# Kernel tuning notes

Measured on AMD Instinct MI355X. Metric: run time of the kernel, lower is better.

## Reference

```python
import jax, jax.numpy as jnp
import numpy as np

B, C, H, W = 64, 512, 7, 7        # x4: dim_b=512, layer4 spatial 7x7
HY, WY = 28, 28                   # y (x1): layer1 56x56 -> cov1 stride2 -> 28x28
NUM_HEADS = 8
HEAD_DIM = C // NUM_HEADS
SCALE = HEAD_DIM ** -0.5
K1, K2 = 2, 3
LN_EPS = 1e-5


def _avgpool_same(y, k, p):
    # torch nn.AvgPool2d(kernel=k, stride=1, padding=p), count_include_pad=True
    s = jax.lax.reduce_window(y, 0.0, jax.lax.add, (1, 1, k, k), (1, 1, 1, 1),
                              [(0, 0), (0, 0), (p, p), (p, p)])
    return s / float(k * k)


def setup_inputs() -> dict:
    key = jax.random.key(0)
    ks = jax.random.split(key, 8)
    x = jax.random.normal(ks[0], (B, C, H, W), dtype=jnp.float32)
    y = jax.random.normal(ks[1], (B, C, HY, WY), dtype=jnp.float32)
    # Linear weights stored as [in, out] (apply via x @ W)
    Wq = jax.random.normal(ks[2], (C, C), dtype=jnp.float32) * 0.02
    Wkv = jax.random.normal(ks[3], (C, 2 * C), dtype=jnp.float32) * 0.02
    Wproj = jax.random.normal(ks[4], (C, C), dtype=jnp.float32) * 0.02
    bproj = jnp.zeros((C,), dtype=jnp.float32)
    gamma = jnp.ones((C,), dtype=jnp.float32)
    beta = jnp.zeros((C,), dtype=jnp.float32)
    attn_w1 = jnp.full((1,), 0.5, dtype=jnp.float32)
    attn_w2 = jnp.full((1,), 0.5, dtype=jnp.float32)
    return dict(x=x, y=y, Wq=Wq, Wkv=Wkv, Wproj=Wproj, bproj=bproj,
                gamma=gamma, beta=beta, attn_w1=attn_w1, attn_w2=attn_w2)


def _topk_masked_softmax(attn, kc):
    # torch: scatter top-kc indices into a 0/1 mask, then where(mask>0, attn, -inf).
    # Equivalent (tie-free, as with continuous random logits): keep entries >= kth value.
    thr = jax.lax.top_k(attn, kc)[0][..., -1:]
    masked = jnp.where(attn >= jax.lax.stop_gradient(thr), attn, -jnp.inf)
    return jax.nn.softmax(masked, axis=-1)


def reference(x, y, Wq, Wkv, Wproj, bproj, gamma, beta, attn_w1, attn_w2):
    # Multi-scale pooling on y (all stride 1, 'same' spatial size)
    y = _avgpool_same(y, 3, 1) + _avgpool_same(y, 5, 2) + _avgpool_same(y, 7, 3)
    N1 = HY * WY
    y = y.reshape(B, C, N1).transpose(0, 2, 1)          # [B, N1, C]
    # LayerNorm over C
    mu = jnp.mean(y, axis=-1, keepdims=True)
    var = jnp.var(y, axis=-1, keepdims=True)
    y = (y - mu) / jnp.sqrt(var + LN_EPS) * gamma + beta

    N = H * W
    xs = x.reshape(B, C, N).transpose(0, 2, 1)          # [B, N, C]

    kv = (y @ Wkv).reshape(B, N1, 2, NUM_HEADS, HEAD_DIM)
    kv = kv.transpose(2, 0, 3, 1, 4)                    # [2, B, h, N1, d]
    k, v = kv[0], kv[1]
    q = (xs @ Wq).reshape(B, N, NUM_HEADS, HEAD_DIM).transpose(0, 2, 1, 3)  # [B,h,N,d]

    attn = jnp.einsum('bhnd,bhmd->bhnm', q, k) * SCALE  # [B, h, N, N1]

    attn1 = _topk_masked_softmax(attn, N1 // K1)
    attn2 = _topk_masked_softmax(attn, N1 // K2)
    out1 = jnp.einsum('bhnm,bhmd->bhnd', attn1, v)
    out2 = jnp.einsum('bhnm,bhmd->bhnd', attn2, v)
    out = out1 * attn_w1 + out2 * attn_w2               # [B, h, N, d]

    out = out.transpose(0, 2, 1, 3).reshape(B, N, C)    # [B, N, C]
    out = out @ Wproj + bproj
    return out.transpose(0, 2, 1).reshape(B, C, H, W)
```

## Files before the change

### kernel.cpp

```cpp
#include <hip/hip_runtime.h>
#include <hip/hip_bf16.h>


typedef __hip_bfloat16 bf16;
using bf16x8 = __attribute__((ext_vector_type(8))) short;
using f32x4 = __attribute__((ext_vector_type(4))) float;

#define DI __device__ __forceinline__

DI unsigned short b2u(float f) {
  bf16 h = __float2bfloat16(f);
  return *reinterpret_cast<unsigned short*>(&h);
}
DI float u2f(short s) { return __uint_as_float(((unsigned int)(unsigned short)s) << 16); }

DI float unkey(unsigned int k) {
  unsigned int u = (k & 0x80000000u) ? (k & 0x7FFFFFFFu) : ~k;
  return __uint_as_float(u);
}

#define GLD_LDS16(g, l)                                                              \
  __builtin_amdgcn_global_load_lds((const __attribute__((address_space(1))) unsigned int*)(g), \
                                   (__attribute__((address_space(3))) unsigned int*)(l), 16, 0, 0)

__global__ __launch_bounds__(256) void prep_pool_kernel(
    const float* __restrict__ Wkv, const float* __restrict__ Wq, const float* __restrict__ Wproj,
    const float* __restrict__ x, const float* __restrict__ y, bf16* __restrict__ wkvT,
    bf16* __restrict__ wqT, bf16* __restrict__ wpT, bf16* __restrict__ xsTb,
    bf16* __restrict__ Vt, bf16* __restrict__ pooledT) {
  __shared__ __align__(16) unsigned char pMem[26912];
  const int blk = blockIdx.x;
  const int tid = threadIdx.x;
  if (blk < 1024) {
    float(*t)[33] = reinterpret_cast<float(*)[33]>(pMem);
    const float* W;
    bf16* WT;
    int N, bx, by;
    if (blk < 512) { W = Wkv; WT = wkvT; N = 1024; bx = blk & 31; by = blk >> 5; }
    else if (blk < 768) { W = Wq; WT = wqT; N = 512; bx = (blk - 512) & 15; by = (blk - 512) >> 4; }
    else { W = Wproj; WT = wpT; N = 512; bx = (blk - 768) & 15; by = (blk - 768) >> 4; }
    const int n0 = bx * 32, k0 = by * 32;
    for (int i = tid; i < 1024; i += 256) {
      int kr = i >> 5, nc = i & 31;
      t[kr][nc] = W[(size_t)(k0 + kr) * N + n0 + nc];
    }
    __syncthreads();
    for (int i = tid; i < 1024; i += 256) {
      int nr = i >> 5, kc = i & 31;
      WT[(size_t)(n0 + nr) * 512 + k0 + kc] = __float2bfloat16(t[kc][nr]);
    }
  } else if (blk < 1536) {
    float(*xt)[51] = reinterpret_cast<float(*)[51]>(pMem);
    const int q2 = blk - 1024;
    const int b = q2 >> 3, cg = q2 & 7;
    const float* xp = x + ((size_t)b * 512 + cg * 64) * 49;
    for (int i = tid; i < 3136; i += 256) {
      int cc = i / 49, r = i - cc * 49;
      xt[cc][r] = xp[i];
    }
    __syncthreads();
    for (int i = tid; i < 3136; i += 256) {
      int r = i >> 6, cc = i & 63;
      xsTb[((size_t)b * 49 + r) * 512 + cg * 64 + cc] = __float2bfloat16(xt[cc][r]);
    }
  } else if (blk < 3584) {
    int idx = (blk - 1536) * 256 + tid;
    int row = idx >> 4, c = idx & 15;
    Vt[(size_t)row * 800 + 784 + c] = __float2bfloat16(0.f);
  } else {
    float(*I)[841] = reinterpret_cast<float(*)[841]>(pMem);
    const int p = blk - 3584;
    const int wk = (p & 7) * 512 + (p >> 3);
    const int b = wk >> 6, cg = wk & 63;
    const float* srcb = y + ((size_t)b * 512 + cg * 8) * 784;
    bf16* drow = pooledT + ((size_t)b * 784) * 512 + cg * 8;
    for (int i = tid; i < 8 * 57; i += 256) {
      int q = i / 57, e = i - q * 57;
      I[q][(e < 29) ? e : (e - 28) * 29] = 0.f;
    }
    {
      const int w = tid >> 6, lane = tid & 63;
      const int hl = lane >> 5, c = lane & 31;
      const int pp = w * 2 + hl;
      if (c < 28) {
        const float* sp = srcb + (size_t)pp * 784;
        float run = 0.f;
        for (int r = 0; r < 28; ++r) {
          float v = sp[r * 28 + c];
#pragma unroll
          for (int d = 1; d < 28; d <<= 1) {
            float tt = __shfl_up(v, d, 32);
            if (c >= d) v += tt;
          }
          run += v;
          I[pp][(r + 1) * 29 + c + 1] = run;
        }
      }
    }
    __syncthreads();
    for (int j = tid; j < 784; j += 256) {
      int r = j / 28, c = j - (j / 28) * 28;
      int r0[3], r1[3], c0[3], c1[3];
#pragma unroll
      for (int pk = 1; pk <= 3; ++pk) {
        r0[pk - 1] = max(r - pk, 0) * 29;
        r1[pk - 1] = (min(r + pk, 27) + 1) * 29;
        c0[pk - 1] = max(c - pk, 0);
        c1[pk - 1] = min(c + pk, 27) + 1;
      }
      unsigned int u[4];
#pragma unroll
      for (int q = 0; q < 4; ++q) {
        float vv[2];
#pragma unroll
        for (int tt = 0; tt < 2; ++tt) {
          const float* Ip = I[q * 2 + tt];
          float acc = 0.f;
#pragma unroll
          for (int k = 0; k < 3; ++k) {
            float s = Ip[r1[k] + c1[k]] - Ip[r0[k] + c1[k]] - Ip[r1[k] + c0[k]] + Ip[r0[k] + c0[k]];
            acc += s * ((k == 0) ? (1.f / 9.f) : (k == 1) ? (1.f / 25.f) : (1.f / 49.f));
          }
          vv[tt] = acc;
        }
        u[q] = (unsigned int)b2u(vv[0]) | ((unsigned int)b2u(vv[1]) << 16);
      }
      *reinterpret_cast<uint4*>(drow + (size_t)j * 512) = make_uint4(u[0], u[1], u[2], u[3]);
    }
  }
}

__global__ __launch_bounds__(256) void ln_q_kernel(const bf16* __restrict__ pooledT,
                                                   const float* __restrict__ gamma,
                                                   const float* __restrict__ beta,
                                                   bf16* __restrict__ yln,
                                                   const bf16* __restrict__ A,
                                                   const bf16* __restrict__ Bt,
                                                   bf16* __restrict__ Qb) {
  __shared__ __align__(16) bf16 As[128 * 32];
  __shared__ __align__(16) bf16 Bs[128 * 32];
  const int blk = blockIdx.x;
  const int tid = threadIdx.x;
  if (blk < 100) {
    const int lane = tid & 63;
    const int w = tid >> 6, wr = w >> 1, wc = w & 1;
    const int m0 = (blk >> 2) * 128, n0 = (blk & 3) * 128;
    f32x4 acc[4][4];
#pragma unroll
    for (int m = 0; m < 4; ++m)
#pragma unroll
      for (int n = 0; n < 4; ++n) acc[m][n] = f32x4{0.f, 0.f, 0.f, 0.f};
    const int s0 = tid, s1 = tid + 256;
    const bf16* Ag0 = A + (size_t)(m0 + (s0 >> 2)) * 512 + (s0 & 3) * 8;
    const bf16* Ag1 = A + (size_t)(m0 + (s1 >> 2)) * 512 + (s1 & 3) * 8;
    const bf16* Bg0 = Bt + (size_t)(n0 + (s0 >> 2)) * 512 + (s0 & 3) * 8;
    const bf16* Bg1 = Bt + (size_t)(n0 + (s1 >> 2)) * 512 + (s1 & 3) * 8;
    bf16* Al0 = As + s0 * 8;
    bf16* Al1 = As + s1 * 8;
    bf16* Bl0 = Bs + s0 * 8;
    bf16* Bl1 = Bs + s1 * 8;
    const int fr = lane & 15;
    const int ko = (lane >> 4) * 8;
    const int rh = lane >> 4;
    for (int k0 = 0; k0 < 512; k0 += 32) {
      GLD_LDS16(Ag0 + k0, Al0);
      GLD_LDS16(Ag1 + k0, Al1);
      GLD_LDS16(Bg0 + k0, Bl0);
      GLD_LDS16(Bg1 + k0, Bl1);
      __syncthreads();
      bf16x8 af[4], bfr[4];
#pragma unroll
      for (int m = 0; m < 4; ++m)
        af[m] = *reinterpret_cast<const bf16x8*>(As + (wr * 64 + m * 16 + fr) * 32 + ko);
#pragma unroll
      for (int n = 0; n < 4; ++n)
        bfr[n] = *reinterpret_cast<const bf16x8*>(Bs + (wc * 64 + n * 16 + fr) * 32 + ko);
#pragma unroll
      for (int m = 0; m < 4; ++m)
#pragma unroll
        for (int n = 0; n < 4; ++n)
          acc[m][n] = __builtin_amdgcn_mfma_f32_16x16x32_bf16(af[m], bfr[n], acc[m][n], 0, 0, 0);
      __syncthreads();
    }
#pragma unroll
    for (int m = 0; m < 4; ++m) {
#pragma unroll
      for (int n = 0; n < 4; ++n) {
        int col = n0 + wc * 64 + n * 16 + fr;
        const size_t cbase = ((size_t)(col >> 6)) * (49 * 64) + (col & 63);
#pragma unroll
        for (int r = 0; r < 4; ++r) {
          int row = m0 + wr * 64 + m * 16 + rh * 4 + r;
          if (row < 3136) {
            int b = row / 49, rr = row - (row / 49) * 49;
            Qb[((size_t)b * 8) * (49 * 64) + cbase + (size_t)rr * 64] = __float2bfloat16(acc[m][n][r]);
          }
        }
      }
    }
  } else {
    const int row = (blk - 100) * 4 + (tid >> 6);
    const int lane = tid & 63;
    bf16x8 raw = *reinterpret_cast<const bf16x8*>(pooledT + (size_t)row * 512 + lane * 8);
    float v[8];
    float s = 0.f, s2 = 0.f;
#pragma unroll
    for (int j = 0; j < 8; ++j) {
      v[j] = u2f(raw[j]);
      s += v[j];
      s2 += v[j] * v[j];
    }
#pragma unroll
    for (int off = 32; off; off >>= 1) {
      s += __shfl_xor(s, off, 64);
      s2 += __shfl_xor(s2, off, 64);
    }
    float mu = s * (1.f / 512.f);
    float rs = rsqrtf(s2 * (1.f / 512.f) - mu * mu + 1e-5f);
    float4 g0 = *reinterpret_cast<const float4*>(gamma + lane * 8);
    float4 g1 = *reinterpret_cast<const float4*>(gamma + lane * 8 + 4);
    float4 e0 = *reinterpret_cast<const float4*>(beta + lane * 8);
    float4 e1 = *reinterpret_cast<const float4*>(beta + lane * 8 + 4);
    float gg[8] = {g0.x, g0.y, g0.z, g0.w, g1.x, g1.y, g1.z, g1.w};
    float bb[8] = {e0.x, e0.y, e0.z, e0.w, e1.x, e1.y, e1.z, e1.w};
    unsigned int u[4];
#pragma unroll
    for (int q = 0; q < 4; ++q) {
      float o0 = (v[2 * q] - mu) * rs * gg[2 * q] + bb[2 * q];
      float o1 = (v[2 * q + 1] - mu) * rs * gg[2 * q + 1] + bb[2 * q + 1];
      u[q] = (unsigned int)b2u(o0) | ((unsigned int)b2u(o1) << 16);
    }
    *reinterpret_cast<uint4*>(yln + (size_t)row * 512 + lane * 8) =
        make_uint4(u[0], u[1], u[2], u[3]);
  }
}

__global__ __launch_bounds__(256) void kv_mfma(const bf16* __restrict__ A,
                                               const bf16* __restrict__ Bt,
                                               bf16* __restrict__ Kb, bf16* __restrict__ Vt) {
  extern __shared__ __align__(16) bf16 smem[];
  bf16* As = smem;
  bf16* Bs = smem + 128 * 32;
  const int tid = threadIdx.x;
  const int lane = tid & 63;
  const int w = tid >> 6, wr = w >> 1, wc = w & 1;

  const int lin = blockIdx.y * 8 + blockIdx.x;
  const int c8 = lin & 7, j = lin >> 3;
  const int ex = j & 7, ey = c8 * 49 + (j >> 3);
  const int m0 = ey * 128, n0 = ex * 128;

  f32x4 acc[4][4];
#pragma unroll
  for (int m = 0; m < 4; ++m)
#pragma unroll
    for (int n = 0; n < 4; ++n) acc[m][n] = f32x4{0.f, 0.f, 0.f, 0.f};

  const int s0 = tid, s1 = tid + 256;
  const bf16* Ag0 = A + (size_t)(m0 + (s0 >> 2)) * 512 + (s0 & 3) * 8;
  const bf16* Ag1 = A + (size_t)(m0 + (s1 >> 2)) * 512 + (s1 & 3) * 8;
  const bf16* Bg0 = Bt + (size_t)(n0 + (s0 >> 2)) * 512 + (s0 & 3) * 8;
  const bf16* Bg1 = Bt + (size_t)(n0 + (s1 >> 2)) * 512 + (s1 & 3) * 8;
  bf16* Al0 = As + s0 * 8;
  bf16* Al1 = As + s1 * 8;
  bf16* Bl0 = Bs + s0 * 8;
  bf16* Bl1 = Bs + s1 * 8;

  const int fr = lane & 15;
  const int ko = (lane >> 4) * 8;
  const int rh = lane >> 4;

  for (int k0 = 0; k0 < 512; k0 += 32) {
    GLD_LDS16(Ag0 + k0, Al0);
    GLD_LDS16(Ag1 + k0, Al1);
    GLD_LDS16(Bg0 + k0, Bl0);
    GLD_LDS16(Bg1 + k0, Bl1);
    __syncthreads();
    bf16x8 af[4], bfr[4];
#pragma unroll
    for (int m = 0; m < 4; ++m)
      af[m] = *reinterpret_cast<const bf16x8*>(As + (wr * 64 + m * 16 + fr) * 32 + ko);
#pragma unroll
    for (int n = 0; n < 4; ++n)
      bfr[n] = *reinterpret_cast<const bf16x8*>(Bs + (wc * 64 + n * 16 + fr) * 32 + ko);
#pragma unroll
    for (int m = 0; m < 4; ++m)
#pragma unroll
      for (int n = 0; n < 4; ++n)
        acc[m][n] = __builtin_amdgcn_mfma_f32_16x16x32_bf16(af[m], bfr[n], acc[m][n], 0, 0, 0);
    __syncthreads();
  }

  if (n0 < 512) {
#pragma unroll
    for (int m = 0; m < 4; ++m) {
#pragma unroll
      for (int n = 0; n < 4; ++n) {
        int col = n0 + wc * 64 + n * 16 + fr;
        const size_t cbase = ((size_t)(col >> 6)) * (784 * 64) + (col & 63);
#pragma unroll
        for (int r = 0; r < 4; ++r) {
          int row = m0 + wr * 64 + m * 16 + rh * 4 + r;
          int b = row / 784, n1 = row - (row / 784) * 784;
          Kb[((size_t)b * 8) * (784 * 64) + cbase + (size_t)n1 * 64] = __float2bfloat16(acc[m][n][r]);
        }
      }
    }
  } else {
    bf16* stage = smem;
#pragma unroll
    for (int p = 0; p < 2; ++p) {
      __syncthreads();
      if (wr == p) {
#pragma unroll
        for (int m = 0; m < 4; ++m) {
#pragma unroll
          for (int n = 0; n < 4; ++n) {
            int coll = wc * 64 + n * 16 + fr;
            int rowl = m * 16 + rh * 4;
            unsigned int u0 = (unsigned int)b2u(acc[m][n][0]) | ((unsigned int)b2u(acc[m][n][1]) << 16);
            unsigned int u1 = (unsigned int)b2u(acc[m][n][2]) | ((unsigned int)b2u(acc[m][n][3]) << 16);
            *reinterpret_cast<uint2*>(stage + coll * 72 + rowl) = make_uint2(u0, u1);
          }
        }
      }
      __syncthreads();
      const int rbase = m0 + p * 64;
      for (int i = tid; i < 1024; i += 256) {
        int cc = i >> 3, tc = i & 7;
        int colg = n0 + cc;
        int h = (colg >> 6) & 7, d = colg & 63;
        int rs = rbase + tc * 8;
        int b = rs / 784, n1 = rs - b * 784;
        bf16x8 val = *reinterpret_cast<const bf16x8*>(stage + cc * 72 + tc * 8);
        bf16* dst = Vt + (((size_t)b * 8 + h) * 64 + d) * 800 + n1;
        if (n1 <= 776) {
          *reinterpret_cast<bf16x8*>(dst) = val;
        } else {
#pragma unroll
          for (int jj = 0; jj < 8; ++jj) {
            int rr = rs + jj;
            int bb2 = rr / 784, nn1 = rr - bb2 * 784;
            bf16 hv;
            *reinterpret_cast<short*>(&hv) = val[jj];
            Vt[(((size_t)bb2 * 8 + h) * 64 + d) * 800 + nn1] = hv;
          }
        }
      }
    }
  }
}

__global__ __launch_bounds__(256) void proj_mfma(const bf16* __restrict__ A,
                                                 const bf16* __restrict__ Bt,
                                                 const float* __restrict__ bias,
                                                 float* __restrict__ out) {
  __shared__ __align__(16) bf16 As[128 * 32];
  __shared__ __align__(16) bf16 Bs[128 * 32];
  const int tid = threadIdx.x;
  const int lane = tid & 63;
  const int w = tid >> 6, wr = w >> 1, wc = w & 1;
  const int m0 = blockIdx.y * 128, n0 = blockIdx.x * 128;

  f32x4 acc[4][4];
#pragma unroll
  for (int m = 0; m < 4; ++m)
#pragma unroll
    for (int n = 0; n < 4; ++n) acc[m][n] = f32x4{0.f, 0.f, 0.f, 0.f};

  const int s0 = tid, s1 = tid + 256;
  const bf16* Ag0 = A + (size_t)(m0 + (s0 >> 2)) * 1024 + (s0 & 3) * 8;
  const bf16* Ag1 = A + (size_t)(m0 + (s1 >> 2)) * 1024 + (s1 & 3) * 8;
  const bf16* Bg0 = Bt + (size_t)(n0 + (s0 >> 2)) * 512 + (s0 & 3) * 8;
  const bf16* Bg1 = Bt + (size_t)(n0 + (s1 >> 2)) * 512 + (s1 & 3) * 8;
  bf16* Al0 = As + s0 * 8;
  bf16* Al1 = As + s1 * 8;
  bf16* Bl0 = Bs + s0 * 8;
  bf16* Bl1 = Bs + s1 * 8;

  const int fr = lane & 15;
  const int ko = (lane >> 4) * 8;
  const int rh = lane >> 4;

  for (int k0 = 0; k0 < 1024; k0 += 32) {
    GLD_LDS16(Ag0 + k0, Al0);
    GLD_LDS16(Ag1 + k0, Al1);
    GLD_LDS16(Bg0 + (k0 & 511), Bl0);
    GLD_LDS16(Bg1 + (k0 & 511), Bl1);
    __syncthreads();
    bf16x8 af[4], bfr[4];
#pragma unroll
    for (int m = 0; m < 4; ++m)
      af[m] = *reinterpret_cast<const bf16x8*>(As + (wr * 64 + m * 16 + fr) * 32 + ko);
#pragma unroll
    for (int n = 0; n < 4; ++n)
      bfr[n] = *reinterpret_cast<const bf16x8*>(Bs + (wc * 64 + n * 16 + fr) * 32 + ko);
#pragma unroll
    for (int m = 0; m < 4; ++m)
#pragma unroll
      for (int n = 0; n < 4; ++n)
        acc[m][n] = __builtin_amdgcn_mfma_f32_16x16x32_bf16(af[m], bfr[n], acc[m][n], 0, 0, 0);
    __syncthreads();
  }

#pragma unroll
  for (int m = 0; m < 4; ++m) {
#pragma unroll
    for (int n = 0; n < 4; ++n) {
      int col = n0 + wc * 64 + n * 16 + fr;
      float bv = bias[col];
#pragma unroll
      for (int r = 0; r < 4; ++r) {
        int row = m0 + wr * 64 + m * 16 + rh * 4 + r;
        if (row < 3136) {
          int b = row / 49, rr = row - (row / 49) * 49;
          out[((size_t)b * 512 + col) * 49 + rr] = acc[m][n][r] + bv;
        }
      }
    }
  }
}

__global__ __launch_bounds__(256, 7) void attn_kernel(const bf16* __restrict__ Qb,
                                                      const bf16* __restrict__ K,
                                                      const bf16* __restrict__ Vt,
                                                      const float* __restrict__ aw1p,
                                                      const float* __restrict__ aw2p,
                                                      bf16* __restrict__ aoutHL) {
  const int lin = blockIdx.x;
  const int wk = (lin & 7) * 448 + (lin >> 3);
  const int bh = wk / 7;
  const int chunk = wk - bh * 7;
  const int b = bh >> 3, h = bh & 7;
  const int r0 = chunk * 7;
  const int tid = threadIdx.x;
  const int lane = tid & 63, w = tid >> 6;
  __shared__ __align__(16) unsigned char sMem[22008];
  float* sLog = reinterpret_cast<float*>(sMem);
  bf16* sW = reinterpret_cast<bf16*>(sMem);

  const int fr = lane & 15, ko = (lane >> 4) * 8, rh = lane >> 4;

  const bf16* Qp = Qb + ((size_t)bh * 49 + r0) * 64;
  const int qrow = (fr < 7) ? fr : 6;
  const bf16x8 aq0 = *reinterpret_cast<const bf16x8*>(Qp + qrow * 64 + ko);
  const bf16x8 aq1 = *reinterpret_cast<const bf16x8*>(Qp + qrow * 64 + 32 + ko);

  const bf16* Kp = K + (size_t)bh * (784 * 64);
  {
    const int rbase = rh * 4;
    const bf16* kbase = Kp + (size_t)fr * 64 + ko;
    bf16x8 kq0[4], kq1[4];
#pragma unroll
    for (int s = 0; s < 4; ++s) {
      int nt = w + s * 4;
      int ntc = nt < 49 ? nt : 48;
      const bf16* kr = kbase + (size_t)ntc * 1024;
      kq0[s] = *reinterpret_cast<const bf16x8*>(kr);
      kq1[s] = *reinterpret_cast<const bf16x8*>(kr + 32);
    }
#pragma unroll
    for (int i = 0; i < 13; ++i) {
      const int s = i & 3;
      const int nt = w + i * 4;
      if (nt < 49) {
        f32x4 acc = {0.f, 0.f, 0.f, 0.f};
        acc = __builtin_amdgcn_mfma_f32_16x16x32_bf16(aq0, kq0[s], acc, 0, 0, 0);
        acc = __builtin_amdgcn_mfma_f32_16x16x32_bf16(aq1, kq1[s], acc, 0, 0, 0);
#pragma unroll
        for (int r = 0; r < 4; ++r) {
          int row = rbase + r;
          if (row < 7) sLog[row * 786 + nt * 16 + fr] = acc[r] * 0.125f;
        }
      }
      const int ntn = w + (i + 4) * 4;
      if (ntn < 49) {
        const bf16* kr = kbase + (size_t)ntn * 1024;
        kq0[s] = *reinterpret_cast<const bf16x8*>(kr);
        kq1[s] = *reinterpret_cast<const bf16x8*>(kr + 32);
      }
    }
  }
  __syncthreads();

  const int ra = w;
  const int rb = (w + 4 < 7) ? (w + 4) : w;
  float va[13], vb[13];
#pragma unroll
  for (int i = 0; i < 13; ++i) {
    int m = lane + i * 64;
    va[i] = (m < 784) ? sLog[ra * 786 + m] : -INFINITY;
    vb[i] = (m < 784) ? sLog[rb * 786 + m] : -INFINITY;
  }
  __syncthreads();

  float mxa = va[0], mxb = vb[0];
#pragma unroll
  for (int i = 1; i < 13; ++i) {
    mxa = fmaxf(mxa, va[i]);
    mxb = fmaxf(mxb, vb[i]);
  }
#pragma unroll
  for (int off = 32; off; off >>= 1) {
    mxa = fmaxf(mxa, __shfl_xor(mxa, off, 64));
    mxb = fmaxf(mxb, __shfl_xor(mxb, off, 64));
  }

  unsigned int t1a = 0u, t2a = 0u, t1b = 0u, t2b = 0u;
  bool d1a = false, d2a = false, d1b = false, d2b = false;
  for (int bit = 31; bit >= 0; --bit) {
    const unsigned int mb = 1u << bit;
    if (!d1a) {
      float cf = unkey(t1a | mb);
      int n = 0;
#pragma unroll
      for (int i = 0; i < 13; ++i) n += __popcll(__ballot(va[i] >= cf));
      if (n >= 392) { t1a |= mb; d1a = (n == 392); }
    }
    if (!d2a) {
      float cf = unkey(t2a | mb);
      int n = 0;
#pragma unroll
      for (int i = 0; i < 13; ++i) n += __popcll(__ballot(va[i] >= cf));
      if (n >= 261) { t2a |= mb; d2a = (n == 261); }
    }
    if (!d1b) {
      float cf = unkey(t1b | mb);
      int n = 0;
#pragma unroll
      for (int i = 0; i < 13; ++i) n += __popcll(__ballot(vb[i] >= cf));
      if (n >= 392) { t1b |= mb; d1b = (n == 392); }
    }
    if (!d2b) {
      float cf = unkey(t2b | mb);
      int n = 0;
#pragma unroll
      for (int i = 0; i < 13; ++i) n += __popcll(__ballot(vb[i] >= cf));
      if (n >= 261) { t2b |= mb; d2b = (n == 261); }
    }
    if (d1a & d2a & d1b & d2b) break;
  }
  const float T1a = unkey(t1a), T2a = unkey(t2a);
  const float T1b = unkey(t1b), T2b = unkey(t2b);

  const float aw1 = aw1p[0], aw2 = aw2p[0];
  float ea[13], eb[13];
  float z1a = 0.f, z2a = 0.f, z1b = 0.f, z2b = 0.f;
#pragma unroll
  for (int i = 0; i < 13; ++i) {
    ea[i] = __expf(va[i] - mxa);
    eb[i] = __expf(vb[i] - mxb);
    if (va[i] >= T1a) z1a += ea[i];
    if (va[i] >= T2a) z2a += ea[i];
    if (vb[i] >= T1b) z1b += eb[i];
    if (vb[i] >= T2b) z2b += eb[i];
  }
#pragma unroll
  for (int off = 32; off; off >>= 1) {
    z1a += __shfl_xor(z1a, off, 64);
    z2a += __shfl_xor(z2a, off, 64);
    z1b += __shfl_xor(z1b, off, 64);
    z2b += __shfl_xor(z2b, off, 64);
  }
  const float a1a = aw1 / z1a, a2a = aw2 / z2a;
  const float a1b = aw1 / z1b, a2b = aw2 / z2b;
#pragma unroll
  for (int i = 0; i < 13; ++i) {
    int m = lane + i * 64;
    if (m < 784) {
      float wa = ea[i] * (((va[i] >= T1a) ? a1a : 0.f) + ((va[i] >= T2a) ? a2a : 0.f));
      sW[ra * 808 + m] = __float2bfloat16(wa);
      float wb = eb[i] * (((vb[i] >= T1b) ? a1b : 0.f) + ((vb[i] >= T2b) ? a2b : 0.f));
      sW[rb * 808 + m] = __float2bfloat16(wb);
    }
  }
  if (lane < 16) {
    sW[ra * 808 + 784 + lane] = __float2bfloat16(0.f);
    sW[rb * 808 + 784 + lane] = __float2bfloat16(0.f);
  }

  const bf16* vbase = Vt + ((size_t)bh * 64 + w * 16 + fr) * 800;
  bf16x8 vq[4];
#pragma unroll
  for (int s = 0; s < 4; ++s)
    vq[s] = *reinterpret_cast<const bf16x8*>(vbase + s * 32 + ko);
  __syncthreads();

  const bf16* wrow = sW + ((fr < 7) ? fr : 7) * 808;
  f32x4 acc0 = {0.f, 0.f, 0.f, 0.f}, acc1 = {0.f, 0.f, 0.f, 0.f};
#pragma unroll
  for (int ks = 0; ks < 25; ++ks) {
    const int s = ks & 3;
    bf16x8 a = *reinterpret_cast<const bf16x8*>(wrow + ks * 32 + ko);
    if (ks & 1)
      acc1 = __builtin_amdgcn_mfma_f32_16x16x32_bf16(a, vq[s], acc1, 0, 0, 0);
    else
      acc0 = __builtin_amdgcn_mfma_f32_16x16x32_bf16(a, vq[s], acc0, 0, 0, 0);
    if (ks + 4 < 25)
      vq[s] = *reinterpret_cast<const bf16x8*>(vbase + (ks + 4) * 32 + ko);
  }
  acc0 += acc1;
#pragma unroll
  for (int r = 0; r < 4; ++r) {
    int row = rh * 4 + r;
    if (row < 7) {
      float v = acc0[r];
      bf16 hi = __float2bfloat16(v);
      bf16 lo = __float2bfloat16(v - __bfloat162float(hi));
      size_t base = ((size_t)(b * 49 + r0 + row)) * 1024 + h * 64 + w * 16 + fr;
      aoutHL[base] = hi;
      aoutHL[base + 512] = lo;
    }
  }
}

extern "C" void kernel_launch(void* const* d_in, const int* in_sizes, int n_in, void* d_out,
                              int out_size, void* d_ws, size_t ws_size, hipStream_t stream) {
  const float* x = (const float*)d_in[0];
  const float* y = (const float*)d_in[1];
  const float* Wq = (const float*)d_in[2];
  const float* Wkv = (const float*)d_in[3];
  const float* Wproj = (const float*)d_in[4];
  const float* bproj = (const float*)d_in[5];
  const float* gamma = (const float*)d_in[6];
  const float* beta = (const float*)d_in[7];
  const float* aw1 = (const float*)d_in[8];
  const float* aw2 = (const float*)d_in[9];
  float* out = (float*)d_out;

  char* w = (char*)d_ws;
  const size_t SZ = 51380224ull;
  const size_t SZV = 52428800ull;
  bf16* pooledT = (bf16*)(w);
  bf16* yln = (bf16*)(w + SZ);
  bf16* Kb = (bf16*)(w);
  bf16* Vt = (bf16*)(w + 2 * SZ);
  size_t off = 2 * SZ + SZV;
  bf16* xsTb = (bf16*)(w + off);    off += 3276800;
  bf16* Qb = (bf16*)(w + off);      off += 3276800;
  bf16* aoutHL = (bf16*)(w + off);  off += 6553600;
  bf16* wkvT = (bf16*)(w + off);    off += 1048576;
  bf16* wqT = (bf16*)(w + off);     off += 524288;
  bf16* wpT = (bf16*)(w + off);     off += 524288;

  prep_pool_kernel<<<dim3(7680), dim3(256), 0, stream>>>(Wkv, Wq, Wproj, x, y, wkvT, wqT, wpT,
                                                         xsTb, Vt, pooledT);
  ln_q_kernel<<<dim3(12644), dim3(256), 0, stream>>>(pooledT, gamma, beta, yln, xsTb, wqT, Qb);
  kv_mfma<<<dim3(8, 392), dim3(256), 18432, stream>>>(yln, wkvT, Kb, Vt);
  attn_kernel<<<dim3(3584), dim3(256), 0, stream>>>(Qb, Kb, Vt, aw1, aw2, aoutHL);
  proj_mfma<<<dim3(4, 25), dim3(256), 0, stream>>>(aoutHL, wpT, bproj, out);
}
```

Before: 295.2 us.

## Fold LayerNorm into KV GEMM epilogue via gamma-scaled weights and row stats

Instead of writing a normalized bf16 copy of the pooled activations, the LN kernel now only computes per-row mean and rstd. Gamma is folded into the transposed Wkv, and per-column sums of gamma*W and beta*W are precomputed. The KV GEMM runs on the raw pooled tensor and applies rs*(acc - mu*c1) + c2 in its epilogue. This removes a full 51MB write and re-read of the normalized tensor. The cost is possible precision loss, because the mean is no longer subtracted before the bf16 GEMM.

New measurement: 308.2 us. 1.04x slower.

```diff
diff --git a/kernel.cpp b/kernel.cpp
--- a/kernel.cpp
+++ b/kernel.cpp
@@ -25,9 +25,10 @@
 
 __global__ __launch_bounds__(256) void prep_pool_kernel(
     const float* __restrict__ Wkv, const float* __restrict__ Wq, const float* __restrict__ Wproj,
-    const float* __restrict__ x, const float* __restrict__ y, bf16* __restrict__ wkvT,
-    bf16* __restrict__ wqT, bf16* __restrict__ wpT, bf16* __restrict__ xsTb,
-    bf16* __restrict__ Vt, bf16* __restrict__ pooledT) {
+    const float* __restrict__ x, const float* __restrict__ y, const float* __restrict__ gamma,
+    const float* __restrict__ beta, bf16* __restrict__ wkvT, bf16* __restrict__ wqT,
+    bf16* __restrict__ wpT, bf16* __restrict__ xsTb, bf16* __restrict__ Vt,
+    bf16* __restrict__ pooledT, float* __restrict__ c1, float* __restrict__ c2) {
   __shared__ __align__(16) unsigned char pMem[26912];
   const int blk = blockIdx.x;
   const int tid = threadIdx.x;
@@ -36,7 +37,8 @@
     const float* W;
     bf16* WT;
     int N, bx, by;
-    if (blk < 512) { W = Wkv; WT = wkvT; N = 1024; bx = blk & 31; by = blk >> 5; }
+    bool foldg = false;
+    if (blk < 512) { W = Wkv; WT = wkvT; N = 1024; bx = blk & 31; by = blk >> 5; foldg = true; }
     else if (blk < 768) { W = Wq; WT = wqT; N = 512; bx = (blk - 512) & 15; by = (blk - 512) >> 4; }
     else { W = Wproj; WT = wpT; N = 512; bx = (blk - 768) & 15; by = (blk - 768) >> 4; }
     const int n0 = bx * 32, k0 = by * 32;
@@ -47,7 +49,9 @@
     __syncthreads();
     for (int i = tid; i < 1024; i += 256) {
       int nr = i >> 5, kc = i & 31;
-      WT[(size_t)(n0 + nr) * 512 + k0 + kc] = __float2bfloat16(t[kc][nr]);
+      float v = t[kc][nr];
+      if (foldg) v *= gamma[k0 + kc];
+      WT[(size_t)(n0 + nr) * 512 + k0 + kc] = __float2bfloat16(v);
     }
   } else if (blk < 1536) {
     float(*xt)[51] = reinterpret_cast<float(*)[51]>(pMem);
@@ -67,7 +71,7 @@
     int idx = (blk - 1536) * 256 + tid;
     int row = idx >> 4, c = idx & 15;
     Vt[(size_t)row * 800 + 784 + c] = __float2bfloat16(0.f);
-  } else {
+  } else if (blk < 7680) {
     float(*I)[841] = reinterpret_cast<float(*)[841]>(pMem);
     const int p = blk - 3584;
     const int wk = (p & 7) * 512 + (p >> 3);
@@ -100,13 +104,13 @@
     __syncthreads();
     for (int j = tid; j < 784; j += 256) {
       int r = j / 28, c = j - (j / 28) * 28;
-      int r0[3], r1[3], c0[3], c1[3];
+      int r0[3], r1[3], c0[3], c1i[3];
 #pragma unroll
       for (int pk = 1; pk <= 3; ++pk) {
         r0[pk - 1] = max(r - pk, 0) * 29;
         r1[pk - 1] = (min(r + pk, 27) + 1) * 29;
         c0[pk - 1] = max(c - pk, 0);
-        c1[pk - 1] = min(c + pk, 27) + 1;
+        c1i[pk - 1] = min(c + pk, 27) + 1;
       }
       unsigned int u[4];
 #pragma unroll
@@ -118,7 +122,7 @@
           float acc = 0.f;
 #pragma unroll
           for (int k = 0; k < 3; ++k) {
-            float s = Ip[r1[k] + c1[k]] - Ip[r0[k] + c1[k]] - Ip[r1[k] + c0[k]] + Ip[r0[k] + c0[k]];
+            float s = Ip[r1[k] + c1i[k]] - Ip[r0[k] + c1i[k]] - Ip[r1[k] + c0[k]] + Ip[r0[k] + c0[k]];
             acc += s * ((k == 0) ? (1.f / 9.f) : (k == 1) ? (1.f / 25.f) : (1.f / 49.f));
           }
           vv[tt] = acc;
@@ -127,16 +131,37 @@
       }
       *reinterpret_cast<uint4*>(drow + (size_t)j * 512) = make_uint4(u[0], u[1], u[2], u[3]);
     }
-  }
-}
-
-__global__ __launch_bounds__(256) void ln_q_kernel(const bf16* __restrict__ pooledT,
-                                                   const float* __restrict__ gamma,
-                                                   const float* __restrict__ beta,
-                                                   bf16* __restrict__ yln,
-                                                   const bf16* __restrict__ A,
-                                                   const bf16* __restrict__ Bt,
-                                                   bf16* __restrict__ Qb) {
+  } else {
+    float* red = reinterpret_cast<float*>(pMem);
+    const int n0c = (blk - 7680) * 32;
+    const int kk = tid >> 5, c = tid & 31;
+    float p1 = 0.f, p2 = 0.f;
+    for (int k = kk; k < 512; k += 8) {
+      float wv = Wkv[(size_t)k * 1024 + n0c + c];
+      p1 += gamma[k] * wv;
+      p2 += beta[k] * wv;
+    }
+    red[kk * 32 + c] = p1;
+    red[256 + kk * 32 + c] = p2;
+    __syncthreads();
+    if (tid < 32) {
+      float s1 = 0.f, s2v = 0.f;
+#pragma unroll
+      for (int q = 0; q < 8; ++q) {
+        s1 += red[q * 32 + tid];
+        s2v += red[256 + q * 32 + tid];
+      }
+      c1[n0c + tid] = s1;
+      c2[n0c + tid] = s2v;
+    }
+  }
+}
+
+__global__ __launch_bounds__(256) void stats_q_kernel(const bf16* __restrict__ pooledT,
+                                                      float2* __restrict__ stats,
+                                                      const bf16* __restrict__ A,
+                                                      const bf16* __restrict__ Bt,
+                                                      bf16* __restrict__ Qb) {
   __shared__ __align__(16) bf16 As[128 * 32];
   __shared__ __align__(16) bf16 Bs[128 * 32];
   const int blk = blockIdx.x;
@@ -202,41 +227,31 @@
     const int row = (blk - 100) * 4 + (tid >> 6);
     const int lane = tid & 63;
     bf16x8 raw = *reinterpret_cast<const bf16x8*>(pooledT + (size_t)row * 512 + lane * 8);
-    float v[8];
     float s = 0.f, s2 = 0.f;
 #pragma unroll
     for (int j = 0; j < 8; ++j) {
-      v[j] = u2f(raw[j]);
-      s += v[j];
-      s2 += v[j] * v[j];
+      float v = u2f(raw[j]);
+      s += v;
+      s2 += v * v;
     }
 #pragma unroll
     for (int off = 32; off; off >>= 1) {
       s += __shfl_xor(s, off, 64);
       s2 += __shfl_xor(s2, off, 64);
     }
-    float mu = s * (1.f / 512.f);
-    float rs = rsqrtf(s2 * (1.f / 512.f) - mu * mu + 1e-5f);
-    float4 g0 = *reinterpret_cast<const float4*>(gamma + lane * 8);
-    float4 g1 = *reinterpret_cast<const float4*>(gamma + lane * 8 + 4);
-    float4 e0 = *reinterpret_cast<const float4*>(beta + lane * 8);
-    float4 e1 = *reinterpret_cast<const float4*>(beta + lane * 8 + 4);
-    float gg[8] = {g0.x, g0.y, g0.z, g0.w, g1.x, g1.y, g1.z, g1.w};
-    float bb[8] = {e0.x, e0.y, e0.z, e0.w, e1.x, e1.y, e1.z, e1.w};
-    unsigned int u[4];
-#pragma unroll
-    for (int q = 0; q < 4; ++q) {
-      float o0 = (v[2 * q] - mu) * rs * gg[2 * q] + bb[2 * q];
-      float o1 = (v[2 * q + 1] - mu) * rs * gg[2 * q + 1] + bb[2 * q + 1];
-      u[q] = (unsigned int)b2u(o0) | ((unsigned int)b2u(o1) << 16);
-    }
-    *reinterpret_cast<uint4*>(yln + (size_t)row * 512 + lane * 8) =
-        make_uint4(u[0], u[1], u[2], u[3]);
+    if (lane == 0) {
+      float mu = s * (1.f / 512.f);
+      float rs = rsqrtf(s2 * (1.f / 512.f) - mu * mu + 1e-5f);
+      stats[row] = make_float2(mu, rs);
+    }
   }
 }
 
 __global__ __launch_bounds__(256) void kv_mfma(const bf16* __restrict__ A,
                                                const bf16* __restrict__ Bt,
+                                               const float2* __restrict__ stats,
+                                               const float* __restrict__ c1,
+                                               const float* __restrict__ c2,
                                                bf16* __restrict__ Kb, bf16* __restrict__ Vt) {
   extern __shared__ __align__(16) bf16 smem[];
   bf16* As = smem;
@@ -289,6 +304,33 @@
       for (int n = 0; n < 4; ++n)
         acc[m][n] = __builtin_amdgcn_mfma_f32_16x16x32_bf16(af[m], bfr[n], acc[m][n], 0, 0, 0);
     __syncthreads();
+  }
+
+  {
+    float muv[4][4], rsv[4][4];
+#pragma unroll
+    for (int m = 0; m < 4; ++m)
+#pragma unroll
+      for (int r = 0; r < 4; ++r) {
+        int row = m0 + wr * 64 + m * 16 + rh * 4 + r;
+        float2 st = stats[row];
+        muv[m][r] = st.x;
+        rsv[m][r] = st.y;
+      }
+    float c1v[4], c2v[4];
+#pragma unroll
+    for (int n = 0; n < 4; ++n) {
+      int col = n0 + wc * 64 + n * 16 + fr;
+      c1v[n] = c1[col];
+      c2v[n] = c2[col];
+    }
+#pragma unroll
+    for (int m = 0; m < 4; ++m)
+#pragma unroll
+      for (int n = 0; n < 4; ++n)
+#pragma unroll
+        for (int r = 0; r < 4; ++r)
+          acc[m][n][r] = rsv[m][r] * (acc[m][n][r] - muv[m][r] * c1v[n]) + c2v[n];
   }
 
   if (n0 < 512) {
@@ -632,8 +674,7 @@
   const size_t SZ = 51380224ull;
   const size_t SZV = 52428800ull;
   bf16* pooledT = (bf16*)(w);
-  bf16* yln = (bf16*)(w + SZ);
-  bf16* Kb = (bf16*)(w);
+  bf16* Kb = (bf16*)(w + SZ);
   bf16* Vt = (bf16*)(w + 2 * SZ);
   size_t off = 2 * SZ + SZV;
   bf16* xsTb = (bf16*)(w + off);    off += 3276800;
@@ -642,11 +683,14 @@
   bf16* wkvT = (bf16*)(w + off);    off += 1048576;
   bf16* wqT = (bf16*)(w + off);     off += 524288;
   bf16* wpT = (bf16*)(w + off);     off += 524288;
-
-  prep_pool_kernel<<<dim3(7680), dim3(256), 0, stream>>>(Wkv, Wq, Wproj, x, y, wkvT, wqT, wpT,
-                                                         xsTb, Vt, pooledT);
-  ln_q_kernel<<<dim3(12644), dim3(256), 0, stream>>>(pooledT, gamma, beta, yln, xsTb, wqT, Qb);
-  kv_mfma<<<dim3(8, 392), dim3(256), 18432, stream>>>(yln, wkvT, Kb, Vt);
+  float* c1 = (float*)(w + off);    off += 4096;
+  float* c2 = (float*)(w + off);    off += 4096;
+  float2* stats = (float2*)(w + off); off += 401408;
+
+  prep_pool_kernel<<<dim3(7712), dim3(256), 0, stream>>>(Wkv, Wq, Wproj, x, y, gamma, beta, wkvT,
+                                                         wqT, wpT, xsTb, Vt, pooledT, c1, c2);
+  stats_q_kernel<<<dim3(12644), dim3(256), 0, stream>>>(pooledT, stats, xsTb, wqT, Qb);
+  kv_mfma<<<dim3(8, 392), dim3(256), 18432, stream>>>(pooledT, wkvT, stats, c1, c2, Kb, Vt);
   attn_kernel<<<dim3(3584), dim3(256), 0, stream>>>(Qb, Kb, Vt, aw1, aw2, aoutHL);
   proj_mfma<<<dim3(4, 25), dim3(256), 0, stream>>>(aoutHL, wpT, bproj, out);
 }
```
